# Optimization experiments

Hardware: AMD Instinct MI355X
Metric: run time of the kernel (lower is better)

The kernel has to match this reference:

```python
import jax, jax.numpy as jnp
import numpy as np

D_MODEL = 1024
NUM_HEADS = 16
MAX_SEQ_LEN = 2048
THETA = 10000.0
D_K = D_MODEL // NUM_HEADS


def setup_inputs() -> dict:
    key = jax.random.key(0)
    ks = jax.random.split(key, 5)
    x = jax.random.normal(ks[0], (2, 2048, D_MODEL), dtype=jnp.float32)
    token_positions = jnp.arange(2048, dtype=jnp.int32)
    s = 1.0 / np.sqrt(D_MODEL)
    w_q = jax.random.normal(ks[1], (D_MODEL, D_MODEL), dtype=jnp.float32) * s
    w_k = jax.random.normal(ks[2], (D_MODEL, D_MODEL), dtype=jnp.float32) * s
    w_v = jax.random.normal(ks[3], (D_MODEL, D_MODEL), dtype=jnp.float32) * s
    w_o = jax.random.normal(ks[4], (D_MODEL, D_MODEL), dtype=jnp.float32) * s
    return {"x": x, "token_positions": token_positions,
            "w_q": w_q, "w_k": w_k, "w_v": w_v, "w_o": w_o}


def _rope_tables():
    inv_freq = 1.0 / (THETA ** (jnp.arange(0, D_K, 2, dtype=jnp.float32) / D_K))
    angles = jnp.arange(MAX_SEQ_LEN, dtype=jnp.float32)[:, None] * inv_freq[None, :]
    return jnp.cos(angles), jnp.sin(angles)  # [max_seq_len, d_k//2]


def _apply_rope(x, cos, sin):
    # x: [..., s, d_k]; interleaved-pair rotation, cos/sin: [s, d_k//2]
    x0 = x[..., 0::2]
    x1 = x[..., 1::2]
    y0 = x0 * cos - x1 * sin
    y1 = x0 * sin + x1 * cos
    return jnp.stack((y0, y1), axis=-1).reshape(x.shape)


def reference(x, token_positions, w_q, w_k, w_v, w_o):
    b, s, _ = x.shape
    h, dk = NUM_HEADS, D_K
    # torch Linear: y = x @ W^T
    q = (x @ w_q.T).reshape(b, s, h, dk).transpose(0, 2, 1, 3)  # [b,h,s,dk]
    k = (x @ w_k.T).reshape(b, s, h, dk).transpose(0, 2, 1, 3)
    v = (x @ w_v.T).reshape(b, s, h, dk).transpose(0, 2, 1, 3)
    cos_c, sin_c = _rope_tables()
    cos = cos_c[token_positions]  # [s, dk//2]
    sin = sin_c[token_positions]
    q = _apply_rope(q, cos, sin)
    k = _apply_rope(k, cos, sin)
    scores = jnp.einsum('bhqd,bhkd->bhqk', q, k) / jnp.sqrt(jnp.float32(dk))
    causal = jnp.tril(jnp.ones((s, s), dtype=bool))
    scores = jnp.where(causal, scores, -jnp.inf)
    attn = jax.nn.softmax(scores, axis=-1)
    out = jnp.einsum('bhqk,bhkd->bhqd', attn, v)
    out = out.transpose(0, 2, 1, 3).reshape(b, s, h * dk)
    return out @ w_o.T
```

## Files before the change

kernel.cpp:

```cpp
#include <hip/hip_runtime.h>
#include <cstdint>
#include <cstddef>

#define DEV static __device__ __forceinline__

typedef __attribute__((ext_vector_type(8))) short bf16x8;
typedef __attribute__((ext_vector_type(4))) float f32x4;

DEV uint16_t f2bf(float f) {
  uint32_t u = __builtin_bit_cast(uint32_t, f);
  u += 0x7FFFu + ((u >> 16) & 1u);
  return (uint16_t)(u >> 16);
}

DEV uint16_t f2bf_trunc(float f) {
  return (uint16_t)(__builtin_bit_cast(uint32_t, f) >> 16);
}

DEV float fexp2(float x) { return __builtin_amdgcn_exp2f(x); }

template <int CTRL>
DEV float dppf(float v) {
  return __builtin_bit_cast(
      float, __builtin_amdgcn_update_dpp(0, __builtin_bit_cast(int, v), CTRL, 0xF, 0xF, true));
}
DEV float rowmax16(float v) {
  v = fmaxf(v, dppf<0xB1>(v));
  v = fmaxf(v, dppf<0x4E>(v));
  v = fmaxf(v, dppf<0x124>(v));
  v = fmaxf(v, dppf<0x128>(v));
  return v;
}
DEV float rowsum16(float v) {
  v += dppf<0xB1>(v);
  v += dppf<0x4E>(v);
  v += dppf<0x124>(v);
  v += dppf<0x128>(v);
  return v;
}

DEV void load_lds16(const void* g, void* l) {
  auto gp = reinterpret_cast<const uint32_t __attribute__((address_space(1)))*>(
      reinterpret_cast<uintptr_t>(g));
  auto lp = reinterpret_cast<uint32_t __attribute__((address_space(3)))*>(
      reinterpret_cast<uintptr_t>(l));
  __builtin_amdgcn_global_load_lds(gp, lp, 16, 0, 0);
}

__global__ __launch_bounds__(256) void cvt_all(const float* __restrict__ x,
                                               const float* __restrict__ wq,
                                               const float* __restrict__ wk,
                                               const float* __restrict__ wv,
                                               const float* __restrict__ wo,
                                               const int* __restrict__ tokpos,
                                               uint16_t* __restrict__ dst,
                                               float2* __restrict__ rtab) {
  int bx = blockIdx.x;
  if (bx >= 8192) {
    int idx = (bx - 8192) * 256 + threadIdx.x;
    int s = idx >> 5, f = idx & 31;
    float invf = __expf(-0.28782314f * (float)f);
    float pos = (float)tokpos[s];
    float sn, cs;
    __sincosf(pos * invf, &sn, &cs);
    rtab[idx] = make_float2(cs, sn);
    return;
  }
  int gi = bx * 1024 + threadIdx.x * 4;
  const float* s;
  int li;
  if (gi < 4194304) {
    s = x; li = gi;
  } else {
    int j = gi - 4194304;
    int r = j >> 20;
    li = j & 1048575;
    s = (r == 0) ? wq : (r == 1) ? wk : (r == 2) ? wv : wo;
  }
  float4 v = *reinterpret_cast<const float4*>(s + li);
  ushort4 o;
  o.x = f2bf(v.x); o.y = f2bf(v.y); o.z = f2bf(v.z); o.w = f2bf(v.w);
  *reinterpret_cast<ushort4*>(dst + gi) = o;
}

__global__ __launch_bounds__(256) void gemm_qkv(const uint16_t* __restrict__ A,
                                                const uint16_t* __restrict__ Wqkv,
                                                uint16_t* __restrict__ QK,
                                                uint16_t* __restrict__ VTb,
                                                const float2* __restrict__ rtab) {
  __shared__ union {
    struct { uint16_t a[2][128 * 64]; uint16_t b[2][128 * 64]; } st;
    uint16_t t[128 * 128];
  } sm;

  const int tid = threadIdx.x;
  const int lane = tid & 63, w = tid >> 6;
  const int q = lane >> 4, l16 = lane & 15;
  const int wm = w & 1, wn = w >> 1;
  const int bm = blockIdx.y, bn = blockIdx.x;
  const int wsel = bn >> 3;

  const f32x4 z4 = {0.f, 0.f, 0.f, 0.f};
  f32x4 acc[4][4];
#pragma unroll
  for (int i = 0; i < 4; ++i)
#pragma unroll
    for (int j = 0; j < 4; ++j) acc[i][j] = z4;

  const int srow = tid >> 3, sslot = tid & 7;
  const uint16_t* Ab = A + (size_t)bm * 128 * 1024;
  const uint16_t* Bb = Wqkv + (size_t)bn * 128 * 1024;

  auto stage = [&](int buf, int k0) {
#pragma unroll
    for (int is = 0; is < 4; ++is) {
      int row = is * 32 + srow;
      int gch = sslot ^ (row & 7);
      char* la = (char*)sm.st.a[buf] + (is * 32 + w * 8) * 128;
      char* lb = (char*)sm.st.b[buf] + (is * 32 + w * 8) * 128;
      load_lds16(Ab + (size_t)row * 1024 + k0 + gch * 8, la);
      load_lds16(Bb + (size_t)row * 1024 + k0 + gch * 8, lb);
    }
  };

  stage(0, 0);
  for (int t = 0; t < 16; ++t) {
    const int cur = t & 1;
    __syncthreads();
    if (t + 1 < 16) stage(cur ^ 1, (t + 1) * 64);
#pragma unroll
    for (int ks = 0; ks < 2; ++ks) {
      bf16x8 af[4], bfr[4];
#pragma unroll
      for (int i = 0; i < 4; ++i) {
        int ra = wm * 64 + i * 16 + l16;
        af[i] = *reinterpret_cast<const bf16x8*>(sm.st.a[cur] + ra * 64 +
                                                 (((ks * 4 + q) ^ (ra & 7)) * 8));
        int rb = wn * 64 + i * 16 + l16;
        bfr[i] = *reinterpret_cast<const bf16x8*>(sm.st.b[cur] + rb * 64 +
                                                  (((ks * 4 + q) ^ (rb & 7)) * 8));
      }
#pragma unroll
      for (int i = 0; i < 4; ++i)
#pragma unroll
        for (int j = 0; j < 4; ++j)
          acc[i][j] =
              __builtin_amdgcn_mfma_f32_16x16x32_bf16(af[i], bfr[j], acc[i][j], 0, 0, 0);
    }
  }

  if (wsel < 2) {
    uint16_t* O = QK + (size_t)wsel * 4194304;
    const float scq = (wsel == 0) ? 0.18033688f : 1.0f;
#pragma unroll
    for (int j = 0; j < 4; ++j) {
      int gn = bn * 128 + wn * 64 + j * 16 + l16;
      int cn = gn & 1023;
      int f = (gn & 63) >> 1;
      float sgn = (lane & 1) ? 1.f : -1.f;
#pragma unroll
      for (int i = 0; i < 4; ++i) {
#pragma unroll
        for (int r = 0; r < 4; ++r) {
          int gm = bm * 128 + wm * 64 + i * 16 + q * 4 + r;
          float2 cssn = rtab[(gm & 2047) * 32 + f];
          float v = acc[i][j][r];
          float o = dppf<0xB1>(v);
          O[(size_t)gm * 1024 + cn] = f2bf((v * cssn.x + sgn * o * cssn.y) * scq);
        }
      }
    }
  } else {
    const int bnv = bn & 7;
    __syncthreads();
#pragma unroll
    for (int i = 0; i < 4; ++i)
#pragma unroll
      for (int j = 0; j < 4; ++j)
#pragma unroll
        for (int r = 0; r < 4; ++r) {
          int mL = wm * 64 + i * 16 + q * 4 + r;
          int nL = wn * 64 + j * 16 + l16;
          int ch = (mL >> 3) ^ (nL & 15);
          sm.t[nL * 128 + ch * 8 + (mL & 7)] = f2bf(acc[i][j][r]);
        }
    __syncthreads();
    const int b = (bm * 128) >> 11;
    const int sblk = (bm * 128) & 2047;
#pragma unroll
    for (int it = 0; it < 8; ++it) {
      int nL = it * 16 + (tid >> 4);
      int mch = tid & 15;
      int slot = mch ^ (nL & 15);
      bf16x8 vv = *reinterpret_cast<const bf16x8*>(sm.t + nL * 128 + slot * 8);
      int gn = bnv * 128 + nL;
      int h = gn >> 6, d = gn & 63;
      *reinterpret_cast<bf16x8*>(VTb + ((size_t)((b * 16 + h) * 64 + d)) * 2048 + sblk +
                                 mch * 8) = vv;
    }
  }
}

__global__ __launch_bounds__(256) void gemm_out(const uint16_t* __restrict__ A,
                                                const uint16_t* __restrict__ Bw,
                                                float* __restrict__ O) {
  __shared__ uint16_t sa[2][128 * 64];
  __shared__ uint16_t sb[2][64 * 64];

  const int tid = threadIdx.x;
  const int lane = tid & 63, w = tid >> 6;
  const int q = lane >> 4, l16 = lane & 15;
  const int bm = blockIdx.y, bn = blockIdx.x;

  const f32x4 z4 = {0.f, 0.f, 0.f, 0.f};
  f32x4 acc[2][4];
#pragma unroll
  for (int i = 0; i < 2; ++i)
#pragma unroll
    for (int j = 0; j < 4; ++j) acc[i][j] = z4;

  const int srow = tid >> 3, sslot = tid & 7;
  const uint16_t* Ab = A + (size_t)bm * 128 * 1024;
  const uint16_t* Bb = Bw + (size_t)bn * 64 * 1024;

  auto stage = [&](int buf, int k0) {
#pragma unroll
    for (int is = 0; is < 4; ++is) {
      int row = is * 32 + srow;
      int gch = sslot ^ (row & 7);
      load_lds16(Ab + (size_t)row * 1024 + k0 + gch * 8,
                 (char*)sa[buf] + (is * 32 + w * 8) * 128);
    }
#pragma unroll
    for (int is = 0; is < 2; ++is) {
      int row = is * 32 + srow;
      int gch = sslot ^ (row & 7);
      load_lds16(Bb + (size_t)row * 1024 + k0 + gch * 8,
                 (char*)sb[buf] + (is * 32 + w * 8) * 128);
    }
  };

  stage(0, 0);
  for (int t = 0; t < 16; ++t) {
    const int cur = t & 1;
    __syncthreads();
    if (t + 1 < 16) stage(cur ^ 1, (t + 1) * 64);
#pragma unroll
    for (int ks = 0; ks < 2; ++ks) {
      bf16x8 af[2], bfr[4];
#pragma unroll
      for (int i = 0; i < 2; ++i) {
        int ra = w * 32 + i * 16 + l16;
        af[i] = *reinterpret_cast<const bf16x8*>(sa[cur] + ra * 64 +
                                                 (((ks * 4 + q) ^ (ra & 7)) * 8));
      }
#pragma unroll
      for (int j = 0; j < 4; ++j) {
        int rb = j * 16 + l16;
        bfr[j] = *reinterpret_cast<const bf16x8*>(sb[cur] + rb * 64 +
                                                  (((ks * 4 + q) ^ (rb & 7)) * 8));
      }
#pragma unroll
      for (int i = 0; i < 2; ++i)
#pragma unroll
        for (int j = 0; j < 4; ++j)
          acc[i][j] =
              __builtin_amdgcn_mfma_f32_16x16x32_bf16(af[i], bfr[j], acc[i][j], 0, 0, 0);
    }
  }

#pragma unroll
  for (int i = 0; i < 2; ++i)
#pragma unroll
    for (int r = 0; r < 4; ++r) {
      int gm = bm * 128 + w * 32 + i * 16 + q * 4 + r;
#pragma unroll
      for (int j = 0; j < 4; ++j) {
        int gn = bn * 64 + j * 16 + l16;
        O[(size_t)gm * 1024 + gn] = acc[i][j][r];
      }
    }
}

__global__ __launch_bounds__(512) void flash_attn(const uint16_t* __restrict__ Q,
                                                  const uint16_t* __restrict__ K,
                                                  const uint16_t* __restrict__ VT,
                                                  uint16_t* __restrict__ AO) {
  __shared__ uint16_t ksm[2][128 * 64];
  __shared__ uint16_t vsm[2][64 * 128];
  __shared__ uint16_t psm[8][16 * 128];

  const int tid = threadIdx.x;
  const int lane = tid & 63, w = tid >> 6;
  const int q = lane >> 4, l16 = lane & 15;
  const int p = blockIdx.x;
  const int bh = blockIdx.y;
  const int b = bh >> 4, h = bh & 15;

  const size_t baseBS = (size_t)b * 2048 * 1024 + h * 64;
  const size_t baseVT = (size_t)bh * 64 * 2048;
  uint16_t* pw = psm[w];
  const f32x4 z4 = {0.f, 0.f, 0.f, 0.f};

  auto stage = [&](int buf, int kt) {
#pragma unroll
    for (int is = 0; is < 2; ++is) {
      int row = is * 64 + (tid >> 3);
      int gch = (tid & 7) ^ (row & 7);
      load_lds16(K + baseBS + (size_t)(kt * 128 + row) * 1024 + gch * 8,
                 (char*)ksm[buf] + (is * 64 + w * 8) * 128);
    }
#pragma unroll
    for (int is = 0; is < 2; ++is) {
      int row = is * 32 + (tid >> 4);
      int gch = (tid & 15) ^ (row & 15);
      load_lds16(VT + baseVT + (size_t)row * 2048 + kt * 128 + gch * 8,
                 (char*)vsm[buf] + (is * 32 + w * 4) * 256);
    }
  };

  for (int t = 0; t < 2; ++t) {
    const int qt = t ? (15 - p) : p;
    const int r0 = qt * 128 + w * 16;
    const int nkt = qt + 1;

    bf16x8 qf[2];
#pragma unroll
    for (int ks = 0; ks < 2; ++ks)
      qf[ks] = *reinterpret_cast<const bf16x8*>(
          Q + baseBS + (size_t)(r0 + l16) * 1024 + ks * 32 + q * 8);

    f32x4 oa[4];
#pragma unroll
    for (int di = 0; di < 4; ++di) oa[di] = z4;
    float m2[4], li[4];
#pragma unroll
    for (int r = 0; r < 4; ++r) { m2[r] = -1e30f; li[r] = 0.f; }

    __syncthreads();
    stage(0, 0);

    for (int kt = 0; kt < nkt; ++kt) {
      const int cur = kt & 1;
      __syncthreads();
      if (kt + 1 < nkt) stage(cur ^ 1, kt + 1);

      f32x4 sc[8];
#pragma unroll
      for (int nj = 0; nj < 8; ++nj) sc[nj] = z4;
#pragma unroll
      for (int ks = 0; ks < 2; ++ks) {
        bf16x8 kf[8];
#pragma unroll
        for (int nj = 0; nj < 8; ++nj) {
          int rk = nj * 16 + l16;
          kf[nj] = *reinterpret_cast<const bf16x8*>(ksm[cur] + rk * 64 +
                                                    (((ks * 4 + q) ^ (rk & 7)) * 8));
        }
#pragma unroll
        for (int nj = 0; nj < 8; ++nj)
          sc[nj] =
              __builtin_amdgcn_mfma_f32_16x16x32_bf16(qf[ks], kf[nj], sc[nj], 0, 0, 0);
      }

      if (kt == nkt - 1) {
#pragma unroll
        for (int nj = 0; nj < 8; ++nj)
#pragma unroll
          for (int r = 0; r < 4; ++r) {
            int col = kt * 128 + nj * 16 + l16;
            int row = r0 + q * 4 + r;
            if (col > row) sc[nj][r] = -1e30f;
          }
      }

      float alpha[4];
#pragma unroll
      for (int r = 0; r < 4; ++r) {
        float v = fmaxf(
            fmaxf(fmaxf(sc[0][r], sc[1][r]), fmaxf(sc[2][r], sc[3][r])),
            fmaxf(fmaxf(sc[4][r], sc[5][r]), fmaxf(sc[6][r], sc[7][r])));
        v = rowmax16(v);
        float mn = fmaxf(m2[r], v);
        alpha[r] = fexp2(m2[r] - mn);
        m2[r] = mn;
        li[r] *= alpha[r];
      }

#pragma unroll
      for (int nj = 0; nj < 8; ++nj)
#pragma unroll
        for (int r = 0; r < 4; ++r) {
          float pv = fexp2(sc[nj][r] - m2[r]);
          li[r] += pv;
          int pr = q * 4 + r;
          int pc = nj * 16 + l16;
          pw[pr * 128 + (((pc >> 3) ^ (pr & 15)) * 8) + (pc & 7)] = f2bf_trunc(pv);
        }

#pragma unroll
      for (int di = 0; di < 4; ++di)
#pragma unroll
        for (int r = 0; r < 4; ++r) oa[di][r] *= alpha[r];

#pragma unroll
      for (int ks = 0; ks < 4; ++ks) {
        bf16x8 pf;
        {
          int pr = l16;
          pf = *reinterpret_cast<const bf16x8*>(pw + pr * 128 +
                                                (((ks * 4 + q) ^ (pr & 15)) * 8));
        }
        bf16x8 vf[4];
#pragma unroll
        for (int di = 0; di < 4; ++di) {
          int vr = di * 16 + l16;
          vf[di] = *reinterpret_cast<const bf16x8*>(vsm[cur] + vr * 128 +
                                                    (((ks * 4 + q) ^ (vr & 15)) * 8));
        }
#pragma unroll
        for (int di = 0; di < 4; ++di)
          oa[di] =
              __builtin_amdgcn_mfma_f32_16x16x32_bf16(pf, vf[di], oa[di], 0, 0, 0);
      }
    }

#pragma unroll
    for (int r = 0; r < 4; ++r) {
      float inv = 1.f / rowsum16(li[r]);
      int gm = r0 + q * 4 + r;
#pragma unroll
      for (int di = 0; di < 4; ++di)
        AO[baseBS + (size_t)gm * 1024 + di * 16 + l16] = f2bf(oa[di][r] * inv);
    }
  }
}

extern "C" void kernel_launch(void* const* d_in, const int* in_sizes, int n_in,
                              void* d_out, int out_size, void* d_ws, size_t ws_size,
                              hipStream_t stream) {
  (void)in_sizes; (void)n_in; (void)out_size; (void)ws_size;
  const float* x = (const float*)d_in[0];
  const int* tokpos = (const int*)d_in[1];
  const float* wq = (const float*)d_in[2];
  const float* wk = (const float*)d_in[3];
  const float* wv = (const float*)d_in[4];
  const float* wo = (const float*)d_in[5];
  float* out = (float*)d_out;

  uint16_t* ws = (uint16_t*)d_ws;
  uint16_t* xb = ws;
  uint16_t* wqb = xb + 4194304;
  uint16_t* wob = wqb + 3145728;
  uint16_t* Qb = wob + 1048576;
  uint16_t* VTb = Qb + 8388608;
  uint16_t* AOb = VTb + 4194304;
  float2* rtab = (float2*)AOb;

  cvt_all<<<8448, 256, 0, stream>>>(x, wq, wk, wv, wo, tokpos, xb, rtab);

  gemm_qkv<<<dim3(24, 32), 256, 0, stream>>>(xb, wqb, Qb, VTb, rtab);

  flash_attn<<<dim3(8, 32), 512, 0, stream>>>(Qb, Qb + 4194304, VTb, AOb);

  gemm_out<<<dim3(16, 32), 256, 0, stream>>>(AOb, wob, out);
}
```

Baseline: 182.2 us.

## Transpose score MFMA, add lazy softmax rescaling, packed P stores, setprio around MFMAs

Swaps the MFMA operands for QK^T so each lane holds scores for a single query row. The row max and sum then need only a few cross-lane ops (swizzle plus bpermute) instead of four DPP reductions per row. The output rescale is skipped unless some row's max grew by more than a threshold of 8 in log2 units, and P is written to LDS as packed 64-bit bf16 stores rather than scalar 16-bit ones. s_setprio raises wave priority around the MFMA blocks. The deferred rescaling depends on exp2 headroom staying bounded, and the masking and swizzle index math was rewritten, so there is some correctness risk.

```diff
diff --git a/kernel.cpp b/kernel.cpp
--- a/kernel.cpp
+++ b/kernel.cpp
@@ -17,6 +17,11 @@
   return (uint16_t)(__builtin_bit_cast(uint32_t, f) >> 16);
 }
 
+DEV uint32_t packbf(float a, float b) {
+  return (__builtin_bit_cast(uint32_t, a) >> 16) |
+         (__builtin_bit_cast(uint32_t, b) & 0xFFFF0000u);
+}
+
 DEV float fexp2(float x) { return __builtin_amdgcn_exp2f(x); }
 
 template <int CTRL>
@@ -24,19 +29,14 @@
   return __builtin_bit_cast(
       float, __builtin_amdgcn_update_dpp(0, __builtin_bit_cast(int, v), CTRL, 0xF, 0xF, true));
 }
-DEV float rowmax16(float v) {
-  v = fmaxf(v, dppf<0xB1>(v));
-  v = fmaxf(v, dppf<0x4E>(v));
-  v = fmaxf(v, dppf<0x124>(v));
-  v = fmaxf(v, dppf<0x128>(v));
-  return v;
-}
-DEV float rowsum16(float v) {
-  v += dppf<0xB1>(v);
-  v += dppf<0x4E>(v);
-  v += dppf<0x124>(v);
-  v += dppf<0x128>(v);
-  return v;
+
+DEV float swz16(float v) {
+  return __builtin_bit_cast(
+      float, __builtin_amdgcn_ds_swizzle(__builtin_bit_cast(int, v), 0x401F));
+}
+DEV float bperm(int lane_idx, float v) {
+  return __builtin_bit_cast(
+      float, __builtin_amdgcn_ds_bpermute(lane_idx << 2, __builtin_bit_cast(int, v)));
 }
 
 DEV void load_lds16(const void* g, void* l) {
@@ -333,9 +333,7 @@
     f32x4 oa[4];
 #pragma unroll
     for (int di = 0; di < 4; ++di) oa[di] = z4;
-    float m2[4], li[4];
-#pragma unroll
-    for (int r = 0; r < 4; ++r) { m2[r] = -1e30f; li[r] = 0.f; }
+    float m2 = -1e30f, li = 0.f;
 
     __syncthreads();
     stage(0, 0);
@@ -357,10 +355,12 @@
           kf[nj] = *reinterpret_cast<const bf16x8*>(ksm[cur] + rk * 64 +
                                                     (((ks * 4 + q) ^ (rk & 7)) * 8));
         }
+        __builtin_amdgcn_s_setprio(1);
 #pragma unroll
         for (int nj = 0; nj < 8; ++nj)
           sc[nj] =
-              __builtin_amdgcn_mfma_f32_16x16x32_bf16(qf[ks], kf[nj], sc[nj], 0, 0, 0);
+              __builtin_amdgcn_mfma_f32_16x16x32_bf16(kf[nj], qf[ks], sc[nj], 0, 0, 0);
+        __builtin_amdgcn_s_setprio(0);
       }
 
       if (kt == nkt - 1) {
@@ -368,40 +368,52 @@
         for (int nj = 0; nj < 8; ++nj)
 #pragma unroll
           for (int r = 0; r < 4; ++r) {
-            int col = kt * 128 + nj * 16 + l16;
-            int row = r0 + q * 4 + r;
+            int col = nj * 16 + q * 4 + r;
+            int row = w * 16 + l16;
             if (col > row) sc[nj][r] = -1e30f;
           }
       }
 
-      float alpha[4];
-#pragma unroll
-      for (int r = 0; r < 4; ++r) {
-        float v = fmaxf(
-            fmaxf(fmaxf(sc[0][r], sc[1][r]), fmaxf(sc[2][r], sc[3][r])),
-            fmaxf(fmaxf(sc[4][r], sc[5][r]), fmaxf(sc[6][r], sc[7][r])));
-        v = rowmax16(v);
-        float mn = fmaxf(m2[r], v);
-        alpha[r] = fexp2(m2[r] - mn);
-        m2[r] = mn;
-        li[r] *= alpha[r];
-      }
-
-#pragma unroll
-      for (int nj = 0; nj < 8; ++nj)
-#pragma unroll
-        for (int r = 0; r < 4; ++r) {
-          float pv = fexp2(sc[nj][r] - m2[r]);
-          li[r] += pv;
-          int pr = q * 4 + r;
-          int pc = nj * 16 + l16;
-          pw[pr * 128 + (((pc >> 3) ^ (pr & 15)) * 8) + (pc & 7)] = f2bf_trunc(pv);
-        }
-
-#pragma unroll
-      for (int di = 0; di < 4; ++di)
-#pragma unroll
-        for (int r = 0; r < 4; ++r) oa[di][r] *= alpha[r];
+      f32x4 m4 = sc[0];
+#pragma unroll
+      for (int nj = 1; nj < 8; ++nj) {
+#pragma unroll
+        for (int r = 0; r < 4; ++r) m4[r] = fmaxf(m4[r], sc[nj][r]);
+      }
+      float pmax = fmaxf(fmaxf(m4[0], m4[1]), fmaxf(m4[2], m4[3]));
+      pmax = fmaxf(pmax, swz16(pmax));
+      pmax = fmaxf(pmax, bperm(lane ^ 32, pmax));
+
+      if (__any(pmax > m2 + 8.f)) {
+        float mn = fmaxf(m2, pmax);
+        float al = fexp2(m2 - mn);
+        m2 = mn;
+        li *= al;
+        float ar[4];
+#pragma unroll
+        for (int r = 0; r < 4; ++r)
+          ar[r] = bperm((lane & 48) | (q * 4 + r), al);
+#pragma unroll
+        for (int di = 0; di < 4; ++di)
+#pragma unroll
+          for (int r = 0; r < 4; ++r) oa[di][r] *= ar[r];
+      }
+
+      {
+        uint16_t* pwr = pw + l16 * 128 + (q & 1) * 4;
+        const int swz = l16 & 15;
+#pragma unroll
+        for (int nj = 0; nj < 8; ++nj) {
+          float e0 = fexp2(sc[nj][0] - m2);
+          float e1 = fexp2(sc[nj][1] - m2);
+          float e2 = fexp2(sc[nj][2] - m2);
+          float e3 = fexp2(sc[nj][3] - m2);
+          li += (e0 + e1) + (e2 + e3);
+          uint64_t pk = (uint64_t)packbf(e0, e1) | ((uint64_t)packbf(e2, e3) << 32);
+          *reinterpret_cast<uint64_t*>(
+              pwr + (((nj * 2 + (q >> 1)) ^ swz) * 8)) = pk;
+        }
+      }
 
 #pragma unroll
       for (int ks = 0; ks < 4; ++ks) {
@@ -418,20 +430,29 @@
           vf[di] = *reinterpret_cast<const bf16x8*>(vsm[cur] + vr * 128 +
                                                     (((ks * 4 + q) ^ (vr & 15)) * 8));
         }
+        __builtin_amdgcn_s_setprio(1);
 #pragma unroll
         for (int di = 0; di < 4; ++di)
           oa[di] =
               __builtin_amdgcn_mfma_f32_16x16x32_bf16(pf, vf[di], oa[di], 0, 0, 0);
-      }
-    }
-
+        __builtin_amdgcn_s_setprio(0);
+      }
+    }
+
+    float lf = li;
+    lf += swz16(lf);
+    lf += bperm(lane ^ 32, lf);
+    float invL = 1.f / lf;
+    float inv_r[4];
+#pragma unroll
+    for (int r = 0; r < 4; ++r)
+      inv_r[r] = bperm((lane & 48) | (q * 4 + r), invL);
 #pragma unroll
     for (int r = 0; r < 4; ++r) {
-      float inv = 1.f / rowsum16(li[r]);
       int gm = r0 + q * 4 + r;
 #pragma unroll
       for (int di = 0; di < 4; ++di)
-        AO[baseBS + (size_t)gm * 1024 + di * 16 + l16] = f2bf(oa[di][r] * inv);
+        AO[baseBS + (size_t)gm * 1024 + di * 16 + l16] = f2bf(oa[di][r] * inv_r[r]);
     }
   }
 }
```

Result: faster. 177.5 us (-2.6%).
